# Kernel tuning notes

Hardware: AMD Instinct MI355X
Metric: run time of the kernel (lower is better)

The kernel has to match this reference:

```python
import jax, jax.numpy as jnp
import numpy as np

HID = 70
NL = 4
NCLS = 10
BN_EPS = 1e-5

def _linear_params(key, din, dout):
    k1, k2 = jax.random.split(key)
    s = 1.0 / np.sqrt(din)
    W = jax.random.uniform(k1, (din, dout), jnp.float32, -s, s)
    b = jax.random.uniform(k2, (dout,), jnp.float32, -s, s)
    return W, b

def setup_inputs():
    key = jax.random.key(0)
    N, E, IN = 100000, 500000, 128
    keys = jax.random.split(key, 64)
    it = iter(keys)
    inp = {}
    inp['h'] = jax.random.normal(next(it), (N, IN), jnp.float32)
    inp['e'] = jax.random.normal(next(it), (E, IN), jnp.float32)
    inp['src'] = jax.random.randint(next(it), (E,), 0, N)
    inp['dst'] = jax.random.randint(next(it), (E,), 0, N)
    inp['snorm_n'] = jax.random.uniform(next(it), (N,), jnp.float32, 0.05, 1.0)
    inp['snorm_e'] = jax.random.uniform(next(it), (E,), jnp.float32, 0.05, 1.0)
    inp['W_eh'], inp['b_eh'] = _linear_params(next(it), IN, HID)
    inp['W_ee'], inp['b_ee'] = _linear_params(next(it), IN, HID)
    for nm in ['A', 'B', 'C', 'D', 'E']:
        Ws, bs = [], []
        for _ in range(NL):
            W, b = _linear_params(next(it), HID, HID)
            Ws.append(W); bs.append(b)
        inp['W' + nm] = jnp.stack(Ws)  # [NL, HID, HID]
        inp['b' + nm] = jnp.stack(bs)  # [NL, HID]
    inp['bnh_g'] = jnp.ones((NL, HID), jnp.float32)
    inp['bnh_b'] = jnp.zeros((NL, HID), jnp.float32)
    inp['bne_g'] = jnp.ones((NL, HID), jnp.float32)
    inp['bne_b'] = jnp.zeros((NL, HID), jnp.float32)
    inp['W_m0'], inp['b_m0'] = _linear_params(next(it), HID, HID // 2)
    inp['W_m1'], inp['b_m1'] = _linear_params(next(it), HID // 2, HID // 4)
    inp['W_m2'], inp['b_m2'] = _linear_params(next(it), HID // 4, NCLS)
    return inp

def _bn(x, g, b):
    # training-mode batch norm over the node/edge dimension
    m = jnp.mean(x, 0)
    v = jnp.var(x, 0)
    return (x - m) * jax.lax.rsqrt(v + BN_EPS) * g + b

def _forward(h, e, snorm_n, snorm_e, W_eh, b_eh, W_ee, b_ee, WA, bA, WB, bB, WC, bC, WD, bD, WE, bE, bnh_g, bnh_b, bne_g, bne_b, W_m0, b_m0, W_m1, b_m1, W_m2, b_m2, src, dst):
    N = h.shape[0]
    snn = snorm_n[:, None]
    sne = snorm_e[:, None]
    h = h @ W_eh + b_eh  # [N, HID]
    e = e @ W_ee + b_ee  # [E, HID]
    for l in range(NL):
        h_in, e_in = h, e
        Ah = h @ WA[l] + bA[l]
        Bh = h @ WB[l] + bB[l]
        Dh = h @ WD[l] + bD[l]
        Eh = h @ WE[l] + bE[l]
        Ce = e @ WC[l] + bC[l]
        e_hat = Ce + Dh[src] + Eh[dst]  # [E, HID] gated edge features
        sigma = jax.nn.sigmoid(e_hat)
        num = jax.ops.segment_sum(sigma * Bh[src], dst, num_segments=N)
        den = jax.ops.segment_sum(sigma, dst, num_segments=N)
        h = Ah + num / (den + 1e-6)
        h = _bn(h * snn, bnh_g[l], bnh_b[l])
        e = _bn(e_hat * sne, bne_g[l], bne_b[l])
        h = h_in + jax.nn.relu(h)  # residual
        e = e_in + jax.nn.relu(e)
    # MLPReadout: 70 -> 35 -> 17 -> n_classes
    y = jax.nn.relu(h @ W_m0 + b_m0)
    y = jax.nn.relu(y @ W_m1 + b_m1)
    return y @ W_m2 + b_m2

def reference(h, e, src, dst, snorm_n, snorm_e, W_eh, b_eh, W_ee, b_ee, WA, bA, WB, bB, WC, bC, WD, bD, WE, bE, bnh_g, bnh_b, bne_g, bne_b, W_m0, b_m0, W_m1, b_m1, W_m2, b_m2):
    return _forward(h, e, snorm_n, snorm_e, W_eh, b_eh, W_ee, b_ee, WA, bA, WB, bB, WC, bC, WD, bD, WE, bE, bnh_g, bnh_b, bne_g, bne_b, W_m0, b_m0, W_m1, b_m1, W_m2, b_m2, src, dst)
```

## Files before the change

kernel.cpp:

```cpp
#include <hip/hip_runtime.h>
#include <math.h>

#define H 70
#define NLAY 4
#define NCLS 10

typedef __attribute__((ext_vector_type(8))) short bf16x8;
typedef __attribute__((ext_vector_type(4))) float f32x4;
typedef __attribute__((ext_vector_type(4))) unsigned int uint4v;
typedef __attribute__((ext_vector_type(4))) int int4v;

struct GemmMats {
    const float* w[4];
    const float* b[4];
    float* y[4];
};

__device__ inline unsigned pack_hi16(unsigned u0, unsigned u1) {
    return (u1 & 0xFFFF0000u) | (u0 >> 16);
}
__device__ inline void split_pair(float x0, float x1, unsigned& ph, unsigned& pl) {
    unsigned u0 = __float_as_uint(x0), u1 = __float_as_uint(x1);
    float l0 = x0 - __uint_as_float(u0 & 0xFFFF0000u);
    float l1 = x1 - __uint_as_float(u1 & 0xFFFF0000u);
    ph = pack_hi16(u0, u1);
    pl = pack_hi16(__float_as_uint(l0), __float_as_uint(l1));
}

template <int K, int KS>
__device__ inline void load_a_frags(const float* __restrict__ X,
                                    const int* __restrict__ perm, int M,
                                    int rowbase, int mlane, int q,
                                    bf16x8* Ah, bf16x8* Al) {
    int rowc = min(rowbase + mlane, M - 1);
    if (perm) rowc = perm[rowc];
    const float* xr = X + (size_t)rowc * K;
#pragma unroll
    for (int ks = 0; ks < KS; ++ks) {
        int k0 = ks * 32 + q * 8;
        float x[8];
        if (k0 + 8 <= K) {
            float2 p0 = *(const float2*)(xr + k0);
            float2 p1 = *(const float2*)(xr + k0 + 2);
            float2 p2 = *(const float2*)(xr + k0 + 4);
            float2 p3 = *(const float2*)(xr + k0 + 6);
            x[0] = p0.x; x[1] = p0.y; x[2] = p1.x; x[3] = p1.y;
            x[4] = p2.x; x[5] = p2.y; x[6] = p3.x; x[7] = p3.y;
        } else {
#pragma unroll
            for (int j = 0; j < 8; ++j) x[j] = (k0 + j < K) ? xr[k0 + j] : 0.f;
        }
        int4v vh, vl;
        unsigned ph, pl;
        split_pair(x[0], x[1], ph, pl); vh.x = ph; vl.x = pl;
        split_pair(x[2], x[3], ph, pl); vh.y = ph; vl.y = pl;
        split_pair(x[4], x[5], ph, pl); vh.z = ph; vl.z = pl;
        split_pair(x[6], x[7], ph, pl); vh.w = ph; vl.w = pl;
        Ah[ks] = __builtin_bit_cast(bf16x8, vh);
        Al[ks] = __builtin_bit_cast(bf16x8, vl);
    }
}

template <int K, int JK, int SW>
__device__ inline void stage_w(const float* __restrict__ Wg, unsigned* Wsh,
                               int tid) {
    for (int idx = tid; idx < 80 * JK; idx += 256) {
        int n = idx / JK, j = idx - n * JK;
        int k0 = 2 * j;
        float w0 = (n < H && k0 < K) ? Wg[k0 * H + n] : 0.f;
        float w1 = (n < H && k0 + 1 < K) ? Wg[(k0 + 1) * H + n] : 0.f;
        unsigned ph, pl;
        split_pair(w0, w1, ph, pl);
        Wsh[n * SW + j] = ph;
        Wsh[80 * SW + n * SW + j] = pl;
    }
}

template <int K, int NMAT>
__global__ __launch_bounds__(256) void gemm_mfma(const float* __restrict__ X,
                                                 const int* __restrict__ perm,
                                                 int M, GemmMats P) {
    constexpr int KS = (K + 31) / 32;
    constexpr int JK = KS * 16;
    constexpr int SW = JK + 4;
    __shared__ unsigned int Wsh[2 * 80 * SW];

    const int tid = threadIdx.x;
    const int wv = tid >> 6;
    const int lane = tid & 63;
    const int mlane = lane & 15;
    const int q = lane >> 4;
    const int rowbase = blockIdx.x * 64 + wv * 16;

    bf16x8 Ah[KS], Al[KS];
    load_a_frags<K, KS>(X, perm, M, rowbase, mlane, q, Ah, Al);

    for (int m = 0; m < NMAT; ++m) {
        __syncthreads();
        stage_w<K, JK, SW>(P.w[m], Wsh, tid);
        __syncthreads();

        f32x4 acc[5];
#pragma unroll
        for (int nt = 0; nt < 5; ++nt) acc[nt] = {0.f, 0.f, 0.f, 0.f};
#pragma unroll
        for (int ks = 0; ks < KS; ++ks) {
#pragma unroll
            for (int nt = 0; nt < 5; ++nt) {
                int base = (nt * 16 + mlane) * SW + ks * 16 + q * 4;
                uint4v bhv = *(const uint4v*)&Wsh[base];
                uint4v blv = *(const uint4v*)&Wsh[80 * SW + base];
                bf16x8 Bhf = __builtin_bit_cast(bf16x8, bhv);
                bf16x8 Blf = __builtin_bit_cast(bf16x8, blv);
                acc[nt] = __builtin_amdgcn_mfma_f32_16x16x32_bf16(Ah[ks], Bhf, acc[nt], 0, 0, 0);
                acc[nt] = __builtin_amdgcn_mfma_f32_16x16x32_bf16(Al[ks], Bhf, acc[nt], 0, 0, 0);
                acc[nt] = __builtin_amdgcn_mfma_f32_16x16x32_bf16(Ah[ks], Blf, acc[nt], 0, 0, 0);
            }
        }
        const float* bm = P.b[m];
        float* Ym = P.y[m];
#pragma unroll
        for (int nt = 0; nt < 5; ++nt) {
            int col = nt * 16 + mlane;
            if (col < H) {
                float bv = bm[col];
#pragma unroll
                for (int r = 0; r < 4; ++r) {
                    int grow = rowbase + q * 4 + r;
                    if (grow < M)
                        Ym[(size_t)grow * H + col] = acc[nt][r] + bv;
                }
            }
        }
    }
}

__global__ __launch_bounds__(256) void gemmC_edge(
    const float* __restrict__ Xe, int E, const float* __restrict__ Wg,
    const float* __restrict__ bias, const float* __restrict__ Dh,
    const float* __restrict__ Eh, const int* __restrict__ src_p,
    const int* __restrict__ dst_p, const float* __restrict__ sne_p,
    float* __restrict__ ehat, float* __restrict__ estats) {
    constexpr int K = 70, KS = 3, JK = 48, SW = 52;
    __shared__ unsigned int Wsh[2 * 80 * SW];
    const int tid = threadIdx.x;
    const int wv = tid >> 6;
    const int lane = tid & 63;
    const int mlane = lane & 15;
    const int q = lane >> 4;

    stage_w<K, JK, SW>(Wg, Wsh, tid);
    __syncthreads();

    float bv[5];
#pragma unroll
    for (int nt = 0; nt < 5; ++nt) {
        int col = nt * 16 + mlane;
        bv[nt] = (col < H) ? bias[col] : 0.f;
    }

    float s1[5] = {0.f, 0.f, 0.f, 0.f, 0.f};
    float s2[5] = {0.f, 0.f, 0.f, 0.f, 0.f};

    const int ntiles = (E + 63) / 64;
    for (int tile = blockIdx.x; tile < ntiles; tile += gridDim.x) {
        const int rowbase = tile * 64 + wv * 16;
        bf16x8 Ah[KS], Al[KS];
        load_a_frags<K, KS>(Xe, nullptr, E, rowbase, mlane, q, Ah, Al);

        f32x4 acc[5];
#pragma unroll
        for (int nt = 0; nt < 5; ++nt) acc[nt] = {0.f, 0.f, 0.f, 0.f};
#pragma unroll
        for (int ks = 0; ks < KS; ++ks) {
#pragma unroll
            for (int nt = 0; nt < 5; ++nt) {
                int base = (nt * 16 + mlane) * SW + ks * 16 + q * 4;
                uint4v bhv = *(const uint4v*)&Wsh[base];
                uint4v blv = *(const uint4v*)&Wsh[80 * SW + base];
                bf16x8 Bhf = __builtin_bit_cast(bf16x8, bhv);
                bf16x8 Blf = __builtin_bit_cast(bf16x8, blv);
                acc[nt] = __builtin_amdgcn_mfma_f32_16x16x32_bf16(Ah[ks], Bhf, acc[nt], 0, 0, 0);
                acc[nt] = __builtin_amdgcn_mfma_f32_16x16x32_bf16(Al[ks], Bhf, acc[nt], 0, 0, 0);
                acc[nt] = __builtin_amdgcn_mfma_f32_16x16x32_bf16(Ah[ks], Blf, acc[nt], 0, 0, 0);
            }
        }
        int s4[4], d4[4];
        float sn4[4];
        bool ok4[4];
#pragma unroll
        for (int r = 0; r < 4; ++r) {
            int grow = rowbase + q * 4 + r;
            bool ok = grow < E;
            int gc = ok ? grow : 0;
            s4[r] = src_p[gc];
            d4[r] = dst_p[gc];
            sn4[r] = sne_p[gc];
            ok4[r] = ok;
        }
#pragma unroll
        for (int nt = 0; nt < 5; ++nt) {
            int col = nt * 16 + mlane;
            if (col < H) {
#pragma unroll
                for (int r = 0; r < 4; ++r) {
                    if (ok4[r]) {
                        int grow = rowbase + q * 4 + r;
                        float v = acc[nt][r] + bv[nt] + Dh[s4[r] * H + col] +
                                  Eh[d4[r] * H + col];
                        ehat[(size_t)grow * H + col] = v;
                        float t = v * sn4[r];
                        s1[nt] += t;
                        s2[nt] += t * t;
                    }
                }
            }
        }
    }
#pragma unroll
    for (int nt = 0; nt < 5; ++nt) {
        s1[nt] += __shfl_xor(s1[nt], 16);
        s1[nt] += __shfl_xor(s1[nt], 32);
        s2[nt] += __shfl_xor(s2[nt], 16);
        s2[nt] += __shfl_xor(s2[nt], 32);
    }
    if (q == 0) {
        float* buf = estats + (size_t)(blockIdx.x & 63) * 140;
#pragma unroll
        for (int nt = 0; nt < 5; ++nt) {
            int col = nt * 16 + mlane;
            if (col < H) {
                unsafeAtomicAdd(&buf[col], s1[nt]);
                unsafeAtomicAdd(&buf[70 + col], s2[nt]);
            }
        }
    }
}

__global__ void count_deg(const int* __restrict__ dst, int E,
                          int* __restrict__ deg) {
    int e = blockIdx.x * 256 + threadIdx.x;
    if (e < E) atomicAdd(&deg[dst[e]], 1);
}

__global__ __launch_bounds__(256) void scan_phaseA(const int* __restrict__ deg,
                                                   int N, int* __restrict__ bsum) {
    __shared__ int red[256];
    int base = blockIdx.x * 1024;
    int s = 0;
    for (int i = threadIdx.x; i < 1024; i += 256) {
        int g = base + i;
        if (g < N) s += deg[g];
    }
    red[threadIdx.x] = s;
    __syncthreads();
    for (int off = 128; off > 0; off >>= 1) {
        if (threadIdx.x < off) red[threadIdx.x] += red[threadIdx.x + off];
        __syncthreads();
    }
    if (threadIdx.x == 0) bsum[blockIdx.x] = red[0];
}

__global__ void scan_phaseB(const int* __restrict__ bsum, int NB,
                            int* __restrict__ boff, int* __restrict__ rowstart,
                            int N) {
    if (threadIdx.x == 0 && blockIdx.x == 0) {
        int acc = 0;
        for (int i = 0; i < NB; ++i) {
            boff[i] = acc;
            acc += bsum[i];
        }
        rowstart[N] = acc;
    }
}

__global__ __launch_bounds__(256) void scan_phaseC(
    const int* __restrict__ deg, int N, const int* __restrict__ boff,
    int* __restrict__ rowstart, int* __restrict__ cursor) {
    __shared__ int thr[256];
    int base = blockIdx.x * 1024 + threadIdx.x * 4;
    int d[4], loc[4];
    int s = 0;
#pragma unroll
    for (int i = 0; i < 4; ++i) {
        int g = base + i;
        d[i] = (g < N) ? deg[g] : 0;
        loc[i] = s;
        s += d[i];
    }
    thr[threadIdx.x] = s;
    __syncthreads();
    if (threadIdx.x == 0) {
        int a = 0;
        for (int i = 0; i < 256; ++i) {
            int t = thr[i];
            thr[i] = a;
            a += t;
        }
    }
    __syncthreads();
    int off = boff[blockIdx.x] + thr[threadIdx.x];
#pragma unroll
    for (int i = 0; i < 4; ++i) {
        int g = base + i;
        if (g < N) {
            rowstart[g] = off + loc[i];
            cursor[g] = off + loc[i];
        }
    }
}

__global__ void csr_fill(const int* __restrict__ dst, int E,
                         int* __restrict__ cursor, int* __restrict__ eid) {
    int e = blockIdx.x * 256 + threadIdx.x;
    if (e < E) {
        int p = atomicAdd(&cursor[dst[e]], 1);
        eid[p] = e;
    }
}

__global__ void perm_build(const int* __restrict__ eid,
                           const int* __restrict__ src,
                           const int* __restrict__ dst,
                           const float* __restrict__ sne, int E,
                           int* __restrict__ src_p, int* __restrict__ dst_p,
                           float* __restrict__ sne_p) {
    int p = blockIdx.x * 256 + threadIdx.x;
    if (p < E) {
        int e = eid[p];
        src_p[p] = src[e];
        dst_p[p] = dst[e];
        sne_p[p] = sne[e];
    }
}

__global__ void bn_finalize_multi(const float* __restrict__ buf, int C,
                                  float inv_cnt, const float* __restrict__ g,
                                  const float* __restrict__ b,
                                  float* __restrict__ scale,
                                  float* __restrict__ shift) {
    __shared__ float red[140];
    int t = threadIdx.x;
    if (t < 140) {
        float s = 0.f;
        for (int i = 0; i < C; ++i) s += buf[(size_t)i * 140 + t];
        red[t] = s;
    }
    __syncthreads();
    if (t < H) {
        float m = red[t] * inv_cnt;
        float v = red[70 + t] * inv_cnt - m * m;
        float rs = rsqrtf(v + 1e-5f);
        float sc = g[t] * rs;
        scale[t] = sc;
        shift[t] = b[t] - m * sc;
    }
}

__global__ __launch_bounds__(256) void node_agg_fused(
    const float* __restrict__ ehat, const float* __restrict__ Bh,
    const float* __restrict__ Ah, const int* __restrict__ src_p,
    const int* __restrict__ rowstart, const float* __restrict__ snn,
    float* __restrict__ e_cur, const float* __restrict__ sne_p,
    const float* __restrict__ escale, const float* __restrict__ eshift, int N,
    float* __restrict__ hpre, float* __restrict__ hstats) {
    const int total = N * H;
    const int stride = gridDim.x * 256;
    int idx0 = blockIdx.x * 256 + threadIdx.x;
    const int c = idx0 % H;
    const float esc = escale[c], esh = eshift[c];
    float s1 = 0.f, s2 = 0.f;
    for (int idx = idx0; idx < total; idx += stride) {
        int n = idx / H;
        int p0 = rowstart[n], p1 = rowstart[n + 1];
        float num = 0.f, den = 0.f;
        for (int p = p0; p < p1; ++p) {
            size_t ei = (size_t)p * H + c;
            float x = ehat[ei];
            float sg = 1.f / (1.f + __expf(-x));
            den += sg;
            int s = src_p[p];
            num = fmaf(sg, Bh[s * H + c], num);
            e_cur[ei] += fmaxf(fmaf(x * sne_p[p], esc, esh), 0.f);
        }
        float val = (Ah[idx] + num / (den + 1e-6f)) * snn[n];
        hpre[idx] = val;
        s1 += val;
        s2 += val * val;
    }
    __shared__ float ls[140];
    for (int i = threadIdx.x; i < 140; i += 256) ls[i] = 0.f;
    __syncthreads();
    atomicAdd(&ls[c], s1);
    atomicAdd(&ls[70 + c], s2);
    __syncthreads();
    float* buf = hstats + (size_t)(blockIdx.x & 15) * 140;
    for (int i = threadIdx.x; i < 140; i += 256) unsafeAtomicAdd(&buf[i], ls[i]);
}

__global__ __launch_bounds__(256) void update_h_kernel(
    float* __restrict__ io, const float* __restrict__ pre,
    const float* __restrict__ scale, const float* __restrict__ shift,
    int total) {
    const int stride = gridDim.x * 256;
    for (int idx = blockIdx.x * 256 + threadIdx.x; idx < total; idx += stride) {
        int r = idx / H;
        int c = idx - r * H;
        io[idx] += fmaxf(fmaf(pre[idx], scale[c], shift[c]), 0.f);
    }
}

__global__ __launch_bounds__(128) void mlp_readout(
    const float* __restrict__ h, int M, const float* __restrict__ W0,
    const float* __restrict__ b0, const float* __restrict__ W1,
    const float* __restrict__ b1, const float* __restrict__ W2,
    const float* __restrict__ b2, float* __restrict__ out) {
    __shared__ float Hs[128 * 71];
    __shared__ float wbuf[70 * 35 + 35 + 35 * 17 + 17 + 17 * 10 + 10];
    float* sW0 = wbuf;
    float* sb0 = sW0 + 2450;
    float* sW1 = sb0 + 35;
    float* sb1 = sW1 + 595;
    float* sW2 = sb1 + 17;
    float* sb2 = sW2 + 170;
    int tid = threadIdx.x;
    for (int i = tid; i < 2450; i += 128) sW0[i] = W0[i];
    for (int i = tid; i < 35; i += 128) sb0[i] = b0[i];
    for (int i = tid; i < 595; i += 128) sW1[i] = W1[i];
    for (int i = tid; i < 17; i += 128) sb1[i] = b1[i];
    for (int i = tid; i < 170; i += 128) sW2[i] = W2[i];
    for (int i = tid; i < 10; i += 128) sb2[i] = b2[i];
    int row0 = blockIdx.x * 128;
    for (int idx = tid; idx < 128 * H; idx += 128) {
        int r = idx / H, k = idx - r * H;
        int g = row0 + r;
        Hs[r * 71 + k] = (g < M) ? h[(size_t)g * H + k] : 0.f;
    }
    __syncthreads();
    int n = row0 + tid;
    if (n < M) {
        float y0[35];
#pragma unroll
        for (int j = 0; j < 35; ++j) y0[j] = sb0[j];
        for (int k = 0; k < H; ++k) {
            float x = Hs[tid * 71 + k];
#pragma unroll
            for (int j = 0; j < 35; ++j) y0[j] = fmaf(x, sW0[k * 35 + j], y0[j]);
        }
#pragma unroll
        for (int j = 0; j < 35; ++j) y0[j] = fmaxf(y0[j], 0.f);
        float y1[17];
#pragma unroll
        for (int j = 0; j < 17; ++j) y1[j] = sb1[j];
        for (int k = 0; k < 35; ++k) {
            float x = y0[k];
#pragma unroll
            for (int j = 0; j < 17; ++j) y1[j] = fmaf(x, sW1[k * 17 + j], y1[j]);
        }
#pragma unroll
        for (int j = 0; j < 17; ++j) y1[j] = fmaxf(y1[j], 0.f);
        float y2[10];
#pragma unroll
        for (int j = 0; j < 10; ++j) y2[j] = sb2[j];
        for (int k = 0; k < 17; ++k) {
            float x = y1[k];
#pragma unroll
            for (int j = 0; j < 10; ++j) y2[j] = fmaf(x, sW2[k * 10 + j], y2[j]);
        }
#pragma unroll
        for (int j = 0; j < 10; ++j) out[(size_t)n * 10 + j] = y2[j];
    }
}

extern "C" void kernel_launch(void* const* d_in, const int* in_sizes, int n_in,
                              void* d_out, int out_size, void* d_ws,
                              size_t ws_size, hipStream_t stream) {
    const float* in_h = (const float*)d_in[0];
    const float* in_e = (const float*)d_in[1];
    const int* src = (const int*)d_in[2];
    const int* dst = (const int*)d_in[3];
    const float* snn = (const float*)d_in[4];
    const float* sne = (const float*)d_in[5];
    const float* W_eh = (const float*)d_in[6];
    const float* b_eh = (const float*)d_in[7];
    const float* W_ee = (const float*)d_in[8];
    const float* b_ee = (const float*)d_in[9];
    const float* WA = (const float*)d_in[10];
    const float* bA = (const float*)d_in[11];
    const float* WB = (const float*)d_in[12];
    const float* bB = (const float*)d_in[13];
    const float* WC = (const float*)d_in[14];
    const float* bC = (const float*)d_in[15];
    const float* WD = (const float*)d_in[16];
    const float* bD = (const float*)d_in[17];
    const float* WE = (const float*)d_in[18];
    const float* bE = (const float*)d_in[19];
    const float* bnh_g = (const float*)d_in[20];
    const float* bnh_b = (const float*)d_in[21];
    const float* bne_g = (const float*)d_in[22];
    const float* bne_b = (const float*)d_in[23];
    const float* W_m0 = (const float*)d_in[24];
    const float* b_m0 = (const float*)d_in[25];
    const float* W_m1 = (const float*)d_in[26];
    const float* b_m1 = (const float*)d_in[27];
    const float* W_m2 = (const float*)d_in[28];
    const float* b_m2 = (const float*)d_in[29];

    const int N = in_sizes[0] / 128;
    const int E = in_sizes[1] / 128;
    const size_t nh = (size_t)N * H;
    const size_t ne = (size_t)E * H;

    float* p = (float*)d_ws;
    float* h_cur = p;   p += nh;
    float* e_cur = p;   p += ne;
    float* Ah = p;      p += nh;
    float* Bh = p;      p += nh;
    float* Dh = p;      p += nh;
    float* Eh = p;      p += nh;
    float* ehat = p;    p += ne;
    float* stats = p;   p += 80 * 140;
    float* escale = p;  p += H;
    float* eshift = p;  p += H;
    float* hscale = p;  p += H;
    float* hshift = p;  p += H;
    float* sne_p = p;   p += E;
    int* ip = (int*)p;
    int* deg = ip;      ip += N;
    int* rowstart = ip; ip += N + 1;
    int* cursor = ip;   ip += N;
    int* eid = ip;      ip += E;
    int* src_p = ip;    ip += E;
    int* dst_p = ip;    ip += E;
    int* bsum = ip;     ip += 256;
    int* boff = ip;     ip += 256;
    float* hpre = Dh;
    float* estats = stats;
    float* hstats = stats + 64 * 140;

    hipMemsetAsync(deg, 0, (size_t)N * sizeof(int), stream);
    count_deg<<<(E + 255) / 256, 256, 0, stream>>>(dst, E, deg);
    const int NB = (N + 1023) / 1024;
    scan_phaseA<<<NB, 256, 0, stream>>>(deg, N, bsum);
    scan_phaseB<<<1, 64, 0, stream>>>(bsum, NB, boff, rowstart, N);
    scan_phaseC<<<NB, 256, 0, stream>>>(deg, N, boff, rowstart, cursor);
    csr_fill<<<(E + 255) / 256, 256, 0, stream>>>(dst, E, cursor, eid);
    perm_build<<<(E + 255) / 256, 256, 0, stream>>>(eid, src, dst, sne, E,
                                                    src_p, dst_p, sne_p);

    GemmMats Ph = {};
    Ph.w[0] = W_eh; Ph.b[0] = b_eh; Ph.y[0] = h_cur;
    gemm_mfma<128, 1><<<(N + 63) / 64, 256, 0, stream>>>(in_h, nullptr, N, Ph);
    GemmMats Pe = {};
    Pe.w[0] = W_ee; Pe.b[0] = b_ee; Pe.y[0] = e_cur;
    gemm_mfma<128, 1><<<(E + 63) / 64, 256, 0, stream>>>(in_e, eid, E, Pe);

    for (int l = 0; l < NLAY; ++l) {
        GemmMats P4;
        P4.w[0] = WA + l * H * H; P4.b[0] = bA + l * H; P4.y[0] = Ah;
        P4.w[1] = WB + l * H * H; P4.b[1] = bB + l * H; P4.y[1] = Bh;
        P4.w[2] = WD + l * H * H; P4.b[2] = bD + l * H; P4.y[2] = Dh;
        P4.w[3] = WE + l * H * H; P4.b[3] = bE + l * H; P4.y[3] = Eh;
        gemm_mfma<70, 4><<<(N + 63) / 64, 256, 0, stream>>>(h_cur, nullptr, N, P4);

        hipMemsetAsync(stats, 0, 80 * 140 * sizeof(float), stream);
        gemmC_edge<<<1024, 256, 0, stream>>>(e_cur, E, WC + l * H * H,
                                             bC + l * H, Dh, Eh, src_p, dst_p,
                                             sne_p, ehat, estats);
        bn_finalize_multi<<<1, 256, 0, stream>>>(estats, 64, 1.f / E,
                                                 bne_g + l * H, bne_b + l * H,
                                                 escale, eshift);
        node_agg_fused<<<1120, 256, 0, stream>>>(ehat, Bh, Ah, src_p, rowstart,
                                                 snn, e_cur, sne_p, escale,
                                                 eshift, N, hpre, hstats);
        bn_finalize_multi<<<1, 256, 0, stream>>>(hstats, 16, 1.f / N,
                                                 bnh_g + l * H, bnh_b + l * H,
                                                 hscale, hshift);
        update_h_kernel<<<2048, 256, 0, stream>>>(h_cur, hpre, hscale, hshift,
                                                  N * H);
    }

    mlp_readout<<<(N + 127) / 128, 128, 0, stream>>>(
        h_cur, N, W_m0, b_m0, W_m1, b_m1, W_m2, b_m2, (float*)d_out);
}
```

Measured before the change: 2.894 ms.

## Defer edge residual BN update into next layer's edge GEMM and vectorize h update

The edge residual update (e += relu(BN(ehat*snorm_e))) is removed from the node aggregation kernel. It is now applied by the next layer's gemmC_edge while it loads e rows, with the updated row written back in place. This takes the strided per-edge read-modify-write of e_cur out of the per-channel aggregation loop and reuses the e and ehat loads the GEMM needs anyway. In the same change, update_h is vectorized with float4 and scale/shift staged in shared memory, the aggregation grid is doubled, and the number of partial stat buffers goes from 16 to 64 to reduce atomic contention. The final layer's edge update is skipped because the output never reads e, and the float4 loads on 70-float rows rely on unaligned global access.

```diff
diff --git a/kernel.cpp b/kernel.cpp
--- a/kernel.cpp
+++ b/kernel.cpp
@@ -25,6 +25,17 @@
     float l1 = x1 - __uint_as_float(u1 & 0xFFFF0000u);
     ph = pack_hi16(u0, u1);
     pl = pack_hi16(__float_as_uint(l0), __float_as_uint(l1));
+}
+
+__device__ inline void split8(const float* x, bf16x8& hi, bf16x8& lo) {
+    int4v vh, vl;
+    unsigned ph, pl;
+    split_pair(x[0], x[1], ph, pl); vh.x = ph; vl.x = pl;
+    split_pair(x[2], x[3], ph, pl); vh.y = ph; vl.y = pl;
+    split_pair(x[4], x[5], ph, pl); vh.z = ph; vl.z = pl;
+    split_pair(x[6], x[7], ph, pl); vh.w = ph; vl.w = pl;
+    hi = __builtin_bit_cast(bf16x8, vh);
+    lo = __builtin_bit_cast(bf16x8, vl);
 }
 
 template <int K, int KS>
@@ -40,24 +51,15 @@
         int k0 = ks * 32 + q * 8;
         float x[8];
         if (k0 + 8 <= K) {
-            float2 p0 = *(const float2*)(xr + k0);
-            float2 p1 = *(const float2*)(xr + k0 + 2);
-            float2 p2 = *(const float2*)(xr + k0 + 4);
-            float2 p3 = *(const float2*)(xr + k0 + 6);
-            x[0] = p0.x; x[1] = p0.y; x[2] = p1.x; x[3] = p1.y;
-            x[4] = p2.x; x[5] = p2.y; x[6] = p3.x; x[7] = p3.y;
+            float4 a0 = *(const float4*)(xr + k0);
+            float4 a1 = *(const float4*)(xr + k0 + 4);
+            x[0] = a0.x; x[1] = a0.y; x[2] = a0.z; x[3] = a0.w;
+            x[4] = a1.x; x[5] = a1.y; x[6] = a1.z; x[7] = a1.w;
         } else {
 #pragma unroll
             for (int j = 0; j < 8; ++j) x[j] = (k0 + j < K) ? xr[k0 + j] : 0.f;
         }
-        int4v vh, vl;
-        unsigned ph, pl;
-        split_pair(x[0], x[1], ph, pl); vh.x = ph; vl.x = pl;
-        split_pair(x[2], x[3], ph, pl); vh.y = ph; vl.y = pl;
-        split_pair(x[4], x[5], ph, pl); vh.z = ph; vl.z = pl;
-        split_pair(x[6], x[7], ph, pl); vh.w = ph; vl.w = pl;
-        Ah[ks] = __builtin_bit_cast(bf16x8, vh);
-        Al[ks] = __builtin_bit_cast(bf16x8, vl);
+        split8(x, Ah[ks], Al[ks]);
     }
 }
 
@@ -136,13 +138,16 @@
 }
 
 __global__ __launch_bounds__(256) void gemmC_edge(
-    const float* __restrict__ Xe, int E, const float* __restrict__ Wg,
-    const float* __restrict__ bias, const float* __restrict__ Dh,
-    const float* __restrict__ Eh, const int* __restrict__ src_p,
-    const int* __restrict__ dst_p, const float* __restrict__ sne_p,
-    float* __restrict__ ehat, float* __restrict__ estats) {
+    float* __restrict__ e_buf, float* __restrict__ ehat, int E,
+    const float* __restrict__ Wg, const float* __restrict__ bias,
+    const float* __restrict__ Dh, const float* __restrict__ Eh,
+    const int* __restrict__ src_p, const int* __restrict__ dst_p,
+    const float* __restrict__ sne_p, const float* __restrict__ escale,
+    const float* __restrict__ eshift, float* __restrict__ estats) {
     constexpr int K = 70, KS = 3, JK = 48, SW = 52;
     __shared__ unsigned int Wsh[2 * 80 * SW];
+    __shared__ float sES[140];
+    const bool first = (escale == nullptr);
     const int tid = threadIdx.x;
     const int wv = tid >> 6;
     const int lane = tid & 63;
@@ -150,6 +155,9 @@
     const int q = lane >> 4;
 
     stage_w<K, JK, SW>(Wg, Wsh, tid);
+    if (!first)
+        for (int i = tid; i < 140; i += 256)
+            sES[i] = (i < 70) ? escale[i] : eshift[i - 70];
     __syncthreads();
 
     float bv[5];
@@ -165,8 +173,55 @@
     const int ntiles = (E + 63) / 64;
     for (int tile = blockIdx.x; tile < ntiles; tile += gridDim.x) {
         const int rowbase = tile * 64 + wv * 16;
-        bf16x8 Ah[KS], Al[KS];
-        load_a_frags<K, KS>(Xe, nullptr, E, rowbase, mlane, q, Ah, Al);
+        const int arow = rowbase + mlane;
+        const bool vrow = arow < E;
+        const int rowc = vrow ? arow : E - 1;
+        const float* er = e_buf + (size_t)rowc * K;
+        const float* hr = ehat + (size_t)rowc * K;
+        float* ew = e_buf + (size_t)rowc * K;
+        const float sn = sne_p[rowc];
+
+        bf16x8 Ahf[KS], Alf[KS];
+#pragma unroll
+        for (int ks = 0; ks < KS; ++ks) {
+            int k0 = ks * 32 + q * 8;
+            float x[8];
+            if (k0 + 8 <= K) {
+                float4 a0 = *(const float4*)(er + k0);
+                float4 a1 = *(const float4*)(er + k0 + 4);
+                x[0] = a0.x; x[1] = a0.y; x[2] = a0.z; x[3] = a0.w;
+                x[4] = a1.x; x[5] = a1.y; x[6] = a1.z; x[7] = a1.w;
+                if (!first) {
+                    float4 h0 = *(const float4*)(hr + k0);
+                    float4 h1 = *(const float4*)(hr + k0 + 4);
+                    float hh[8] = {h0.x, h0.y, h0.z, h0.w,
+                                   h1.x, h1.y, h1.z, h1.w};
+#pragma unroll
+                    for (int j = 0; j < 8; ++j)
+                        x[j] += fmaxf(
+                            fmaf(hh[j] * sn, sES[k0 + j], sES[70 + k0 + j]),
+                            0.f);
+                    if (vrow) {
+                        *(float4*)(ew + k0) =
+                            make_float4(x[0], x[1], x[2], x[3]);
+                        *(float4*)(ew + k0 + 4) =
+                            make_float4(x[4], x[5], x[6], x[7]);
+                    }
+                }
+            } else {
+#pragma unroll
+                for (int j = 0; j < 8; ++j) {
+                    int kk = k0 + j;
+                    x[j] = (kk < K) ? er[kk] : 0.f;
+                    if (!first && kk < K) {
+                        x[j] += fmaxf(
+                            fmaf(hr[kk] * sn, sES[kk], sES[70 + kk]), 0.f);
+                        if (vrow) ew[kk] = x[j];
+                    }
+                }
+            }
+            split8(x, Ahf[ks], Alf[ks]);
+        }
 
         f32x4 acc[5];
 #pragma unroll
@@ -180,9 +235,9 @@
                 uint4v blv = *(const uint4v*)&Wsh[80 * SW + base];
                 bf16x8 Bhf = __builtin_bit_cast(bf16x8, bhv);
                 bf16x8 Blf = __builtin_bit_cast(bf16x8, blv);
-                acc[nt] = __builtin_amdgcn_mfma_f32_16x16x32_bf16(Ah[ks], Bhf, acc[nt], 0, 0, 0);
-                acc[nt] = __builtin_amdgcn_mfma_f32_16x16x32_bf16(Al[ks], Bhf, acc[nt], 0, 0, 0);
-                acc[nt] = __builtin_amdgcn_mfma_f32_16x16x32_bf16(Ah[ks], Blf, acc[nt], 0, 0, 0);
+                acc[nt] = __builtin_amdgcn_mfma_f32_16x16x32_bf16(Ahf[ks], Bhf, acc[nt], 0, 0, 0);
+                acc[nt] = __builtin_amdgcn_mfma_f32_16x16x32_bf16(Alf[ks], Bhf, acc[nt], 0, 0, 0);
+                acc[nt] = __builtin_amdgcn_mfma_f32_16x16x32_bf16(Ahf[ks], Blf, acc[nt], 0, 0, 0);
             }
         }
         int s4[4], d4[4];
@@ -357,31 +412,25 @@
     }
 }
 
-__global__ __launch_bounds__(256) void node_agg_fused(
+__global__ __launch_bounds__(256) void node_agg2(
     const float* __restrict__ ehat, const float* __restrict__ Bh,
     const float* __restrict__ Ah, const int* __restrict__ src_p,
-    const int* __restrict__ rowstart, const float* __restrict__ snn,
-    float* __restrict__ e_cur, const float* __restrict__ sne_p,
-    const float* __restrict__ escale, const float* __restrict__ eshift, int N,
+    const int* __restrict__ rowstart, const float* __restrict__ snn, int N,
     float* __restrict__ hpre, float* __restrict__ hstats) {
     const int total = N * H;
     const int stride = gridDim.x * 256;
     int idx0 = blockIdx.x * 256 + threadIdx.x;
     const int c = idx0 % H;
-    const float esc = escale[c], esh = eshift[c];
     float s1 = 0.f, s2 = 0.f;
     for (int idx = idx0; idx < total; idx += stride) {
         int n = idx / H;
         int p0 = rowstart[n], p1 = rowstart[n + 1];
         float num = 0.f, den = 0.f;
         for (int p = p0; p < p1; ++p) {
-            size_t ei = (size_t)p * H + c;
-            float x = ehat[ei];
+            float x = ehat[(size_t)p * H + c];
             float sg = 1.f / (1.f + __expf(-x));
             den += sg;
-            int s = src_p[p];
-            num = fmaf(sg, Bh[s * H + c], num);
-            e_cur[ei] += fmaxf(fmaf(x * sne_p[p], esc, esh), 0.f);
+            num = fmaf(sg, Bh[src_p[p] * H + c], num);
         }
         float val = (Ah[idx] + num / (den + 1e-6f)) * snn[n];
         hpre[idx] = val;
@@ -394,19 +443,33 @@
     atomicAdd(&ls[c], s1);
     atomicAdd(&ls[70 + c], s2);
     __syncthreads();
-    float* buf = hstats + (size_t)(blockIdx.x & 15) * 140;
+    float* buf = hstats + (size_t)(blockIdx.x & 63) * 140;
     for (int i = threadIdx.x; i < 140; i += 256) unsafeAtomicAdd(&buf[i], ls[i]);
 }
 
-__global__ __launch_bounds__(256) void update_h_kernel(
+__global__ __launch_bounds__(256) void update_h4(
     float* __restrict__ io, const float* __restrict__ pre,
     const float* __restrict__ scale, const float* __restrict__ shift,
-    int total) {
+    int total4) {
+    __shared__ float sS[70], sB[70];
+    for (int i = threadIdx.x; i < 70; i += 256) {
+        sS[i] = scale[i];
+        sB[i] = shift[i];
+    }
+    __syncthreads();
     const int stride = gridDim.x * 256;
-    for (int idx = blockIdx.x * 256 + threadIdx.x; idx < total; idx += stride) {
-        int r = idx / H;
-        int c = idx - r * H;
-        io[idx] += fmaxf(fmaf(pre[idx], scale[c], shift[c]), 0.f);
+    for (int idx = blockIdx.x * 256 + threadIdx.x; idx < total4; idx += stride) {
+        float4 pv = ((const float4*)pre)[idx];
+        float4 iv = ((float4*)io)[idx];
+        int c0 = (idx * 4) % 70;
+        int c1 = c0 + 1; if (c1 >= 70) c1 -= 70;
+        int c2 = c0 + 2; if (c2 >= 70) c2 -= 70;
+        int c3 = c0 + 3; if (c3 >= 70) c3 -= 70;
+        iv.x += fmaxf(fmaf(pv.x, sS[c0], sB[c0]), 0.f);
+        iv.y += fmaxf(fmaf(pv.y, sS[c1], sB[c1]), 0.f);
+        iv.z += fmaxf(fmaf(pv.z, sS[c2], sB[c2]), 0.f);
+        iv.w += fmaxf(fmaf(pv.w, sS[c3], sB[c3]), 0.f);
+        ((float4*)io)[idx] = iv;
     }
 }
 
@@ -519,7 +582,7 @@
     float* Dh = p;      p += nh;
     float* Eh = p;      p += nh;
     float* ehat = p;    p += ne;
-    float* stats = p;   p += 80 * 140;
+    float* stats = p;   p += 128 * 140;
     float* escale = p;  p += H;
     float* eshift = p;  p += H;
     float* hscale = p;  p += H;
@@ -563,21 +626,21 @@
         P4.w[3] = WE + l * H * H; P4.b[3] = bE + l * H; P4.y[3] = Eh;
         gemm_mfma<70, 4><<<(N + 63) / 64, 256, 0, stream>>>(h_cur, nullptr, N, P4);
 
-        hipMemsetAsync(stats, 0, 80 * 140 * sizeof(float), stream);
-        gemmC_edge<<<1024, 256, 0, stream>>>(e_cur, E, WC + l * H * H,
-                                             bC + l * H, Dh, Eh, src_p, dst_p,
-                                             sne_p, ehat, estats);
+        hipMemsetAsync(stats, 0, 128 * 140 * sizeof(float), stream);
+        gemmC_edge<<<1024, 256, 0, stream>>>(
+            e_cur, ehat, E, WC + l * H * H, bC + l * H, Dh, Eh, src_p, dst_p,
+            sne_p, (l == 0) ? nullptr : escale, (l == 0) ? nullptr : eshift,
+            estats);
         bn_finalize_multi<<<1, 256, 0, stream>>>(estats, 64, 1.f / E,
                                                  bne_g + l * H, bne_b + l * H,
                                                  escale, eshift);
-        node_agg_fused<<<1120, 256, 0, stream>>>(ehat, Bh, Ah, src_p, rowstart,
-                                                 snn, e_cur, sne_p, escale,
-                                                 eshift, N, hpre, hstats);
-        bn_finalize_multi<<<1, 256, 0, stream>>>(hstats, 16, 1.f / N,
+        node_agg2<<<2240, 256, 0, stream>>>(ehat, Bh, Ah, src_p, rowstart, snn,
+                                            N, hpre, hstats);
+        bn_finalize_multi<<<1, 256, 0, stream>>>(hstats, 64, 1.f / N,
                                                  bnh_g + l * H, bnh_b + l * H,
                                                  hscale, hshift);
-        update_h_kernel<<<2048, 256, 0, stream>>>(h_cur, hpre, hscale, hshift,
-                                                  N * H);
+        update_h4<<<2048, 256, 0, stream>>>(h_cur, hpre, hscale, hshift,
+                                            (N * H) / 4);
     }
 
     mlp_readout<<<(N + 127) / 128, 128, 0, stream>>>(
```

Result: no change. 2.938 ms (+1.5%).
